# Optimization experiments

Hardware: AMD Instinct MI355X
Metric: run time of the kernel (lower is better)

## Reference

```python
import jax, jax.numpy as jnp
import numpy as np

DIM = 256
HEADS = 8
DIM_HEAD = 64
HIDDEN = HEADS * DIM_HEAD
SCALE = DIM_HEAD ** -0.5


def setup_inputs() -> dict:
    key = jax.random.key(0)
    ks = jax.random.split(key, 8)
    std = 0.02
    x = jax.random.normal(ks[0], (2, DIM, 16, 64, 64), dtype=jnp.float32)
    Wq = jax.random.normal(ks[1], (HIDDEN, DIM), dtype=jnp.float32) * std
    Wk = jax.random.normal(ks[2], (HIDDEN, DIM), dtype=jnp.float32) * std
    Wv = jax.random.normal(ks[3], (HIDDEN, DIM), dtype=jnp.float32) * std
    Wg = jax.random.normal(ks[4], (HIDDEN, DIM), dtype=jnp.float32) * std
    bg = jnp.zeros((HIDDEN,), dtype=jnp.float32)
    Wo = jax.random.normal(ks[5], (DIM, HIDDEN), dtype=jnp.float32) * std
    bo = jnp.zeros((DIM,), dtype=jnp.float32)
    return {"x": x, "Wq": Wq, "Wk": Wk, "Wv": Wv, "Wg": Wg, "bg": bg, "Wo": Wo, "bo": bo}


def _proj(x, W):  # 1x1 conv, no bias: (B,C,H,W) @ (O,C) -> (B,O,H,W)
    return jnp.einsum('bchw,oc->bohw', x, W)


def reference(x, Wq, Wk, Wv, Wg, bg, Wo, bo):
    b, c, f, h, w = x.shape
    xf = x.transpose(0, 2, 1, 3, 4).reshape(b * f, c, h, w)  # (bf, c, h, w)
    q = _proj(xf, Wq)
    k = _proj(xf, Wk)
    v = _proj(xf, Wv)
    g = _proj(xf, Wg) + bg[None, :, None, None]
    # softmax over height for q, width for k (pre-reshape, as in torch)
    q = jax.nn.softmax(q, axis=-2)
    k = jax.nn.softmax(k, axis=-1)

    def to_heads(t):  # (bf, H*D, h, w) -> (bf, H, h*w, D)
        return t.reshape(b * f, HEADS, DIM_HEAD, h * w).transpose(0, 1, 3, 2)

    q, k, v, g = map(to_heads, (q, k, v, g))
    q = jax.nn.elu(q) + 1.0
    k = jax.nn.elu(k) + 1.0
    g = jax.nn.sigmoid(g)

    kv = jnp.einsum('bhnd,bhne->bhde', k, v)
    k_sum = k.sum(axis=2)                                   # (bf, H, D)
    z = 1.0 / jnp.maximum(jnp.einsum('bhnd,bhd->bhn', q, k_sum), 1e-6)
    out = jnp.einsum('bhnd,bhde->bhne', q * SCALE, kv)
    out = out * z[..., None] * g                            # (bf, H, n, D)

    out = out.transpose(0, 1, 3, 2).reshape(b * f, HIDDEN, h, w)
    out = jnp.einsum('bchw,oc->bohw', out, Wo) + bo[None, :, None, None]
    return out.reshape(b, f, c, h, w).transpose(0, 2, 1, 3, 4)
```

## Files before the change

kernel.cpp:

```cpp
#include <hip/hip_runtime.h>


typedef unsigned short u16;
typedef unsigned int u32;
typedef __bf16 bf16x8 __attribute__((ext_vector_type(8)));
typedef float f32x4 __attribute__((ext_vector_type(4)));

typedef const __attribute__((address_space(1))) void* gas_t;
typedef __attribute__((address_space(3))) void* las_t;
__device__ __forceinline__ void gll16(const void* g, void* l) {
    __builtin_amdgcn_global_load_lds((gas_t)g, (las_t)l, 16, 0, 0);
}

__device__ inline float bf2f(u16 v) { union { u32 i; float f; } u; u.i = ((u32)v) << 16; return u.f; }
__device__ inline u16 f2bf(float f) {
    union { float f; u32 i; } u; u.f = f;
    u32 r = (u.i + 0x7fffu + ((u.i >> 16) & 1u)) >> 16;
    return (u16)r;
}
__device__ inline void split2(float v, u16& h, u16& l) {
    h = f2bf(v);
    l = f2bf(v - bf2f(h));
}

__global__ void k_cvt_w(const float* __restrict__ Wq, const float* __restrict__ Wk,
                        const float* __restrict__ Wv, const float* __restrict__ Wg,
                        const float* __restrict__ Wo,
                        u16* __restrict__ Wh, u16* __restrict__ Wl,
                        u16* __restrict__ Woh, u16* __restrict__ Wol)
{
    int idx = blockIdx.x * 256 + threadIdx.x;
    if (idx < 524288) {
        int o = idx >> 8, c = idx & 255;
        int which = o >> 9, r = o & 511;
        const float* s = (which == 0) ? Wq : (which == 1) ? Wk : (which == 2) ? Wv : Wg;
        u16 h, l; split2(s[r * 256 + c], h, l);
        Wh[idx] = h; Wl[idx] = l;
    } else {
        int j = idx - 524288;
        if (j < 131072) { u16 h, l; split2(Wo[j], h, l); Woh[j] = h; Wol[j] = l; }
    }
}

__global__ __launch_bounds__(256) void k_cvt_x(const float* __restrict__ x,
                                               u16* __restrict__ xh, u16* __restrict__ xl,
                                               int c0)
{
    __shared__ __align__(16) u16 tileh[64 * 132];
    __shared__ __align__(16) u16 tilel[64 * 132];
    const int t = threadIdx.x;
    const int bfl = blockIdx.y;
    const int bfg = c0 + bfl;
    const int n0 = blockIdx.x * 128;
    const int b_ = bfg >> 4, f_ = bfg & 15;
    for (int s = 0; s < 2; ++s) {
        for (int ch2 = 0; ch2 < 2; ++ch2) {
            __syncthreads();
            for (int p = 0; p < 8; ++p) {
                int cl = p * 16 + (t >> 4);
                int c = ch2 * 128 + cl;
                const float* sp = x + (((size_t)b_ * 256 + c) * 16 + f_) * 4096
                                    + n0 + s * 64 + (t & 15) * 4;
                float4 v = *(const float4*)sp;
                float vv[4] = { v.x, v.y, v.z, v.w };
#pragma unroll
                for (int j = 0; j < 4; ++j) {
                    int nl = (t & 15) * 4 + j;
                    u16 h, l; split2(vv[j], h, l);
                    tileh[nl * 132 + cl] = h;
                    tilel[nl * 132 + cl] = l;
                }
            }
            __syncthreads();
#pragma unroll
            for (int i = 0; i < 4; ++i) {
                int flat = t + i * 256;
                int nn = flat >> 4, cc = flat & 15;
                size_t off = ((size_t)bfl * 4096 + n0 + s * 64 + nn) * 256 + ch2 * 128 + cc * 8;
                *(uint4*)(xh + off) = *(const uint4*)(tileh + nn * 132 + cc * 8);
                *(uint4*)(xl + off) = *(const uint4*)(tilel + nn * 132 + cc * 8);
            }
        }
    }
}

__global__ __launch_bounds__(256) void k_proj(
    const u16* __restrict__ Wh, const u16* __restrict__ Wl,
    const u16* __restrict__ xh, const u16* __restrict__ xl,
    const float* __restrict__ bg,
    float* __restrict__ qf,
    u16* __restrict__ kh, u16* __restrict__ kl,
    u16* __restrict__ vh, u16* __restrict__ vl,
    float* __restrict__ gf)
{
    __shared__ __align__(16) char smem[65536];
    u16* Ah = (u16*)smem;
    u16* Al = (u16*)(smem + 16384);
    u16* Bh = (u16*)(smem + 32768);
    u16* Bl = (u16*)(smem + 49152);
    float* Csh = (float*)smem;
    const int t = threadIdx.x;
    const int bfl = blockIdx.z;
    const int by = blockIdx.y;
    const int m0 = (by < 4) ? by * 128 : 512 + (by - 4) * 128;
    const int n0 = blockIdx.x * 128;
    const int lane = t & 63, wv = t >> 6, wm = wv >> 1, wn = wv & 1;
    f32x4 acc[4][4] = {};
    const u16* Aph = Wh + (size_t)m0 * 256;
    const u16* Apl = Wl + (size_t)m0 * 256;
    const u16* Bph = xh + ((size_t)bfl * 4096 + n0) * 256;
    const u16* Bpl = xl + ((size_t)bfl * 4096 + n0) * 256;

    for (int kt = 0; kt < 4; ++kt) {
        const int k0 = kt * 64;
#pragma unroll
        for (int jj = 0; jj < 4; ++jj) {
            int s = wv * 4 + jj;
            int row = s * 8 + (lane >> 3);
            int csrc = (lane & 7) ^ (row & 7);
            size_t go = (size_t)row * 256 + k0 + csrc * 8;
            gll16(Aph + go, Ah + s * 512);
            gll16(Apl + go, Al + s * 512);
            gll16(Bph + go, Bh + s * 512);
            gll16(Bpl + go, Bl + s * 512);
        }
        __syncthreads();
#pragma unroll
        for (int kk = 0; kk < 2; ++kk) {
            bf16x8 afh[4], afl[4], bfh[4], bfl_[4];
#pragma unroll
            for (int i = 0; i < 4; ++i) {
                int ra = wm * 64 + i * 16 + (lane & 15);
                int ca = ((kk * 4 + (lane >> 4)) ^ (ra & 7)) * 8;
                afh[i] = *(const bf16x8*)(Ah + ra * 64 + ca);
                afl[i] = *(const bf16x8*)(Al + ra * 64 + ca);
                int rb = wn * 64 + i * 16 + (lane & 15);
                int cb = ((kk * 4 + (lane >> 4)) ^ (rb & 7)) * 8;
                bfh[i] = *(const bf16x8*)(Bh + rb * 64 + cb);
                bfl_[i] = *(const bf16x8*)(Bl + rb * 64 + cb);
            }
#pragma unroll
            for (int mi = 0; mi < 4; ++mi)
#pragma unroll
                for (int ni = 0; ni < 4; ++ni) {
                    acc[mi][ni] = __builtin_amdgcn_mfma_f32_16x16x32_bf16(afh[mi], bfh[ni], acc[mi][ni], 0, 0, 0);
                    acc[mi][ni] = __builtin_amdgcn_mfma_f32_16x16x32_bf16(afh[mi], bfl_[ni], acc[mi][ni], 0, 0, 0);
                    acc[mi][ni] = __builtin_amdgcn_mfma_f32_16x16x32_bf16(afl[mi], bfh[ni], acc[mi][ni], 0, 0, 0);
                }
        }
        __syncthreads();
    }

    const int sector = m0 >> 9;
    for (int ph = 0; ph < 2; ++ph) {
        if (wn == ph) {
#pragma unroll
            for (int mi = 0; mi < 4; ++mi)
#pragma unroll
                for (int ni = 0; ni < 4; ++ni)
#pragma unroll
                    for (int r = 0; r < 4; ++r) {
                        int gr = wm * 64 + mi * 16 + (lane >> 4) * 4 + r;
                        int gcl = ni * 16 + (lane & 15);
                        Csh[gr * 69 + gcl] = acc[mi][ni][r];
                    }
        }
        __syncthreads();
        if (sector == 0) {
#pragma unroll
            for (int rr = 0; rr < 2; ++rr) {
                int n_loc = rr * 32 + (t >> 3);
                int oct = t & 7;
                float* dst = qf + ((size_t)bfl * 4096 + n0 + ph * 64 + n_loc) * 512 + m0;
#pragma unroll
                for (int j = 0; j < 4; ++j) {
                    f32x4 o;
#pragma unroll
                    for (int c = 0; c < 4; ++c)
                        o[c] = Csh[(j * 32 + oct * 4 + c) * 69 + n_loc];
                    *(f32x4*)(dst + j * 32 + oct * 4) = o;
                }
            }
        } else if (t < 128) {
            const float* src = Csh + t * 69;
            const int oloc = (m0 & 511) + t;
            const size_t doff = ((size_t)bfl * 512 + oloc) * 4096 + n0 + ph * 64;
            if (sector == 2) {
#pragma unroll
                for (int i = 0; i < 8; ++i) {
                    union { u16 h[8]; uint4 u; } ph_, pl_;
#pragma unroll
                    for (int j = 0; j < 8; ++j) split2(src[i * 8 + j], ph_.h[j], pl_.h[j]);
                    *(uint4*)(vh + doff + i * 8) = ph_.u;
                    *(uint4*)(vl + doff + i * 8) = pl_.u;
                }
            } else if (sector == 1) {
                float mx = -3.0e38f;
                for (int j = 0; j < 64; ++j) mx = fmaxf(mx, src[j]);
                float sum = 0.f;
                for (int j = 0; j < 64; ++j) sum += expf(src[j] - mx);
                float rs = 1.0f / sum;
#pragma unroll
                for (int i = 0; i < 8; ++i) {
                    union { u16 h[8]; uint4 u; } ph_, pl_;
#pragma unroll
                    for (int j = 0; j < 8; ++j) {
                        float p = expf(src[i * 8 + j] - mx) * rs;
                        split2(p, ph_.h[j], pl_.h[j]);
                    }
                    *(uint4*)(kh + doff + i * 8) = ph_.u;
                    *(uint4*)(kl + doff + i * 8) = pl_.u;
                }
            } else {
                float bgv = bg[oloc];
#pragma unroll
                for (int i = 0; i < 16; ++i) {
                    float4 o;
                    float* po = (float*)&o;
#pragma unroll
                    for (int j = 0; j < 4; ++j)
                        po[j] = 1.0f / (1.0f + expf(-(src[i * 4 + j] + bgv)));
                    *(float4*)(gf + doff + i * 4) = o;
                }
            }
        }
        __syncthreads();
    }
}

__global__ __launch_bounds__(256) void k_smq(
    const float* __restrict__ qf, u16* __restrict__ qTh, u16* __restrict__ qTl)
{
    __shared__ float S[4 * 64 * 64];
    const int t = threadIdx.x;
    const int wblk = blockIdx.x;
    const int bh = blockIdx.y;
    const int bfl = bh >> 3, head = bh & 7;
    const float* qbase = qf + (size_t)bfl * 4096 * 512 + head * 64;
#pragma unroll
    for (int r = 0; r < 16; ++r) {
        int h = r * 4 + (t >> 6);
        int w = (t >> 4) & 3;
        int li = t & 15;
        f32x4 v = *(const f32x4*)(qbase + (size_t)(h * 64 + wblk * 4 + w) * 512 + li * 4);
        *(f32x4*)(S + ((w * 64 + h) * 64 + li * 4)) = v;
    }
    __syncthreads();
    {
        int w = t >> 6, d = t & 63;
        float mx = -3.0e38f;
        for (int h = 0; h < 64; ++h) mx = fmaxf(mx, S[(w * 64 + h) * 64 + d]);
        float sum = 0.f;
        for (int h = 0; h < 64; ++h) {
            int i = (w * 64 + h) * 64 + d;
            float e = expf(S[i] - mx);
            S[i] = e;
            sum += e;
        }
        float rs = 1.0f / sum;
        for (int h = 0; h < 64; ++h) S[(w * 64 + h) * 64 + d] *= rs;
    }
    __syncthreads();
#pragma unroll
    for (int r = 0; r < 8; ++r) {
        int px = r * 32 + (t >> 3);
        int h = px >> 2, w = px & 3;
        int oct = t & 7;
        union { u16 h16[8]; uint4 u; } ph_, pl_;
#pragma unroll
        for (int j = 0; j < 8; ++j)
            split2(S[(w * 64 + h) * 64 + oct * 8 + j], ph_.h16[j], pl_.h16[j]);
        size_t off = ((size_t)bh * 4096 + h * 64 + wblk * 4 + w) * 64 + oct * 8;
        *(uint4*)(qTh + off) = ph_.u;
        *(uint4*)(qTl + off) = pl_.u;
    }
}

__global__ __launch_bounds__(256) void k_kv(
    const u16* __restrict__ kh, const u16* __restrict__ kl,
    const u16* __restrict__ vh, const u16* __restrict__ vl,
    float* __restrict__ kvp, float* __restrict__ vsp, float* __restrict__ ksp)
{
    __shared__ __align__(16) char smem[65536];
    u16* Kh = (u16*)smem;
    u16* Kl = (u16*)(smem + 16384);
    u16* Vh = (u16*)(smem + 32768);
    u16* Vl = (u16*)(smem + 49152);
    float* mrg = (float*)smem;
    const int t = threadIdx.x;
    const int oct = blockIdx.x;
    const int bh = blockIdx.y;
    const int NBH = gridDim.y;
    const int lane = t & 63, wv = t >> 6;
    const size_t hb = (size_t)bh * 64 * 4096;

    f32x4 acc[5][5] = {};
    bf16x8 ones;
#pragma unroll
    for (int j = 0; j < 8; ++j) ones[j] = (lane & 15) == 0 ? (__bf16)1.0f : (__bf16)0.0f;

    for (int cc = 0; cc < 4; ++cc) {
        const int pxc = oct * 512 + cc * 128;
#pragma unroll
        for (int jj = 0; jj < 4; ++jj) {
            int s = wv * 4 + jj;
            int row = s * 4 + (lane >> 4);
            int csrc = (lane & 15) ^ (row & 7);
            size_t go = hb + (size_t)row * 4096 + pxc + csrc * 8;
            gll16(kh + go, Kh + s * 512);
            gll16(kl + go, Kl + s * 512);
            gll16(vh + go, Vh + s * 512);
            gll16(vl + go, Vl + s * 512);
        }
        __syncthreads();
        bf16x8 ah[4], al[4], bh_[4], bl_[4];
#pragma unroll
        for (int i = 0; i < 4; ++i) {
            int ra = i * 16 + (lane & 15);
            int kc = (wv * 4 + (lane >> 4)) ^ (ra & 7);
            int off = ra * 128 + kc * 8;
            ah[i]  = *(const bf16x8*)(Kh + off);
            al[i]  = *(const bf16x8*)(Kl + off);
            bh_[i] = *(const bf16x8*)(Vh + off);
            bl_[i] = *(const bf16x8*)(Vl + off);
        }
#pragma unroll
        for (int di = 0; di < 5; ++di) {
            bf16x8 a = (di < 4) ? ah[di] : ones;
#pragma unroll
            for (int ei = 0; ei < 5; ++ei) {
                bf16x8 b = (ei < 4) ? bh_[ei] : ones;
                acc[di][ei] = __builtin_amdgcn_mfma_f32_16x16x32_bf16(a, b, acc[di][ei], 0, 0, 0);
            }
        }
#pragma unroll
        for (int di = 0; di < 5; ++di) {
            bf16x8 a = (di < 4) ? ah[di] : ones;
#pragma unroll
            for (int ei = 0; ei < 4; ++ei)
                acc[di][ei] = __builtin_amdgcn_mfma_f32_16x16x32_bf16(a, bl_[ei], acc[di][ei], 0, 0, 0);
        }
#pragma unroll
        for (int di = 0; di < 4; ++di)
#pragma unroll
            for (int ei = 0; ei < 5; ++ei) {
                bf16x8 b = (ei < 4) ? bh_[ei] : ones;
                acc[di][ei] = __builtin_amdgcn_mfma_f32_16x16x32_bf16(al[di], b, acc[di][ei], 0, 0, 0);
            }
        __syncthreads();
    }

    float* kvm = mrg;
    float* vsm = mrg + 64 * 68;
    float* ksm = mrg + 64 * 68 + 64;
    for (int i = t; i < 64 * 68 + 128; i += 256) mrg[i] = 0.f;
    __syncthreads();
#pragma unroll
    for (int di = 0; di < 4; ++di)
#pragma unroll
        for (int ei = 0; ei < 4; ++ei)
#pragma unroll
            for (int r = 0; r < 4; ++r) {
                int d = di * 16 + (lane >> 4) * 4 + r;
                int e = ei * 16 + (lane & 15);
                atomicAdd(&kvm[d * 68 + e], acc[di][ei][r]);
            }
    if (lane < 16) {
#pragma unroll
        for (int ei = 0; ei < 4; ++ei) atomicAdd(&vsm[ei * 16 + lane], acc[4][ei][0]);
    }
    if ((lane & 15) == 0) {
#pragma unroll
        for (int di = 0; di < 4; ++di)
#pragma unroll
            for (int r = 0; r < 4; ++r)
                atomicAdd(&ksm[di * 16 + (lane >> 4) * 4 + r], acc[di][4][r]);
    }
    __syncthreads();
    float* op = kvp + ((size_t)oct * NBH + bh) * 4096;
#pragma unroll
    for (int i = 0; i < 16; ++i) {
        int idx = t + i * 256;
        op[idx] = kvm[(idx >> 6) * 68 + (idx & 63)];
    }
    if (t < 64) {
        vsp[((size_t)oct * NBH + bh) * 64 + t] = vsm[t];
        ksp[((size_t)oct * NBH + bh) * 64 + t] = 512.0f + ksm[t];
    }
}

__global__ __launch_bounds__(256) void k_merge(
    const float* __restrict__ kvp, const float* __restrict__ vsp,
    const float* __restrict__ ksp,
    u16* __restrict__ kvTh, u16* __restrict__ kvTl,
    float* __restrict__ aux, int NBH)
{
    __shared__ float kv[64 * 68];
    __shared__ float vsl[64];
    __shared__ float kslL[64];
    const int t = threadIdx.x;
    const int bh = blockIdx.x;
#pragma unroll
    for (int i = 0; i < 16; ++i) {
        int idx = t + i * 256;
        float s = 0.f;
#pragma unroll
        for (int o = 0; o < 8; ++o) s += kvp[((size_t)o * NBH + bh) * 4096 + idx];
        kv[(idx >> 6) * 68 + (idx & 63)] = s;
    }
    if (t < 64) {
        float a = 0.f, b = 0.f;
#pragma unroll
        for (int o = 0; o < 8; ++o) {
            a += vsp[((size_t)o * NBH + bh) * 64 + t];
            b += ksp[((size_t)o * NBH + bh) * 64 + t];
        }
        vsl[t] = a; kslL[t] = b;
    }
    __syncthreads();
    if (t < 64) {
        float s = 0.f;
        for (int d = 0; d < 64; ++d) s += kv[d * 68 + t];
        aux[(size_t)bh * 68 + t] = s + 64.0f * vsl[t];
    }
    if (t == 64) {
        float s = 0.f;
        for (int d = 0; d < 64; ++d) s += kslL[d];
        aux[(size_t)bh * 68 + 64] = s;
    }
    __syncthreads();
    {
        int m = t >> 2, kq = t & 3;
        union { u16 h[16]; uint4 u[2]; } hh, ll;
        float vm = vsl[m];
#pragma unroll
        for (int i = 0; i < 16; ++i) {
            int k = kq * 16 + i;
            split2(kv[k * 68 + m] + vm, hh.h[i], ll.h[i]);
        }
        size_t off = (size_t)bh * 5120 + (size_t)m * 64 + kq * 16;
        *(uint4*)(kvTh + off) = hh.u[0];
        *(uint4*)(kvTh + off + 8) = hh.u[1];
        *(uint4*)(kvTl + off) = ll.u[0];
        *(uint4*)(kvTl + off + 8) = ll.u[1];
    }
    if (t < 64) {
        int m2 = 64 + (t >> 2), kq = t & 3;
        union { u16 h[16]; uint4 u[2]; } hh, ll;
#pragma unroll
        for (int i = 0; i < 16; ++i) {
            float v = (m2 == 64) ? kslL[kq * 16 + i] : 0.f;
            split2(v, hh.h[i], ll.h[i]);
        }
        size_t off = (size_t)bh * 5120 + (size_t)m2 * 64 + kq * 16;
        *(uint4*)(kvTh + off) = hh.u[0];
        *(uint4*)(kvTh + off + 8) = hh.u[1];
        *(uint4*)(kvTl + off) = ll.u[0];
        *(uint4*)(kvTl + off + 8) = ll.u[1];
    }
}

__global__ __launch_bounds__(256) void k_att(
    const u16* __restrict__ qTh_g, const u16* __restrict__ qTl_g,
    const float* __restrict__ gf,
    const u16* __restrict__ kvTh_g, const u16* __restrict__ kvTl_g,
    const float* __restrict__ aux,
    u16* __restrict__ atth, u16* __restrict__ attl)
{
    __shared__ __align__(16) char smem[71680];
    u16* qh_s = (u16*)smem;
    u16* ql_s = (u16*)(smem + 32768);
    u16* ah_s = (u16*)smem;
    u16* al_s = (u16*)(smem + 34816);
    float* szl = (float*)(smem + 69632);
    float* cslL = (float*)(smem + 70656);
    const int t = threadIdx.x;
    const int lane = t & 63, wv = t >> 6;
    const int row = lane & 15, oct = lane >> 4;
    const int bh = blockIdx.y;
    const int bfl = bh >> 3, head = bh & 7;
    const int n0 = blockIdx.x * 256;

    const u16* qhb = qTh_g + ((size_t)bh * 4096 + n0) * 64;
    const u16* qlb = qTl_g + ((size_t)bh * 4096 + n0) * 64;
#pragma unroll
    for (int r = 0; r < 8; ++r) {
        int chunk = r * 256 + t;
        int n = chunk >> 3, c = chunk & 7;
        size_t src = (size_t)n * 64 + (size_t)((c ^ (n & 7)) * 8);
        gll16(qhb + src, qh_s + r * 2048 + wv * 512);
        gll16(qlb + src, ql_s + r * 2048 + wv * 512);
    }
    if (t < 65) cslL[t] = aux[(size_t)bh * 68 + t];
    __syncthreads();

    f32x4 acc[5][4] = {};
    const u16* Ahg = kvTh_g + (size_t)bh * 5120;
    const u16* Alg = kvTl_g + (size_t)bh * 5120;
#pragma unroll
    for (int pass = 0; pass < 3; ++pass) {
        const u16* Ap = (pass == 2) ? Alg : Ahg;
        const u16* Bp = (pass == 1) ? ql_s : qh_s;
#pragma unroll
        for (int ks = 0; ks < 2; ++ks) {
            bf16x8 af[5], bq[4];
#pragma unroll
            for (int mi = 0; mi < 5; ++mi)
                af[mi] = *(const bf16x8*)(Ap + (size_t)(mi * 16 + row) * 64 + ks * 32 + oct * 8);
#pragma unroll
            for (int ni = 0; ni < 4; ++ni) {
                int n_loc = wv * 64 + ni * 16 + row;
                int chs = ((ks * 4 + oct) ^ (n_loc & 7)) * 8;
                bq[ni] = *(const bf16x8*)(Bp + n_loc * 64 + chs);
            }
#pragma unroll
            for (int mi = 0; mi < 5; ++mi)
#pragma unroll
                for (int ni = 0; ni < 4; ++ni)
                    acc[mi][ni] = __builtin_amdgcn_mfma_f32_16x16x32_bf16(af[mi], bq[ni], acc[mi][ni], 0, 0, 0);
        }
    }
    if (oct == 0) {
#pragma unroll
        for (int ni = 0; ni < 4; ++ni)
            szl[wv * 64 + ni * 16 + row] = acc[4][ni][0];
    }
    __syncthreads();

    const float kstp = cslL[64];
#pragma unroll
    for (int ni = 0; ni < 4; ++ni) {
        int n_loc = wv * 64 + ni * 16 + row;
        int n_g = n0 + n_loc;
        float zz = 0.125f / fmaxf(szl[n_loc] + kstp, 1e-6f);
#pragma unroll
        for (int mi = 0; mi < 4; ++mi) {
            int e0 = mi * 16 + oct * 4;
            u16 hh[4], ll2[4];
#pragma unroll
            for (int r2 = 0; r2 < 4; ++r2) {
                int e = e0 + r2;
                float g = gf[((size_t)bfl * 512 + head * 64 + e) * 4096 + n_g];
                float val = (acc[mi][ni][r2] + cslL[e]) * zz * g;
                split2(val, hh[r2], ll2[r2]);
            }
            *(u32*)(ah_s + n_loc * 68 + e0)     = (u32)hh[0] | ((u32)hh[1] << 16);
            *(u32*)(ah_s + n_loc * 68 + e0 + 2) = (u32)hh[2] | ((u32)hh[3] << 16);
            *(u32*)(al_s + n_loc * 68 + e0)     = (u32)ll2[0] | ((u32)ll2[1] << 16);
            *(u32*)(al_s + n_loc * 68 + e0 + 2) = (u32)ll2[2] | ((u32)ll2[3] << 16);
        }
    }
    __syncthreads();
    u16* gh = atth + ((size_t)bfl * 4096 + n0) * 512 + head * 64;
    u16* gl = attl + ((size_t)bfl * 4096 + n0) * 512 + head * 64;
#pragma unroll
    for (int r = 0; r < 16; ++r) {
        int n_loc = r * 16 + (t >> 4);
        int u2 = t & 15;
        *(uint2*)(gh + (size_t)n_loc * 512 + u2 * 4) = *(const uint2*)(ah_s + n_loc * 68 + u2 * 4);
        *(uint2*)(gl + (size_t)n_loc * 512 + u2 * 4) = *(const uint2*)(al_s + n_loc * 68 + u2 * 4);
    }
}

__global__ __launch_bounds__(256) void k_out(
    const u16* __restrict__ Woh, const u16* __restrict__ Wol,
    const u16* __restrict__ atth, const u16* __restrict__ attl,
    const float* __restrict__ bo, float* __restrict__ out, int c0)
{
    __shared__ __align__(16) u16 smem[32768];
    u16* Ah = smem;
    u16* Al = smem + 8192;
    u16* Bh = smem + 16384;
    u16* Bl = smem + 24576;
    const int t = threadIdx.x;
    const int bfl = blockIdx.z;
    const int bfg = c0 + bfl;
    const int m0 = blockIdx.y * 128;
    const int n0 = blockIdx.x * 128;
    const int lane = t & 63, wv = t >> 6, wm = wv >> 1, wn = wv & 1;
    f32x4 acc[4][4] = {};
    const u16* Aph = Woh + (size_t)m0 * 512;
    const u16* Apl = Wol + (size_t)m0 * 512;
    const u16* Bph = atth + ((size_t)bfl * 4096 + n0) * 512;
    const u16* Bpl = attl + ((size_t)bfl * 4096 + n0) * 512;
    for (int kt = 0; kt < 8; ++kt) {
        const int k0 = kt * 64;
#pragma unroll
        for (int jj = 0; jj < 4; ++jj) {
            int s = wv * 4 + jj;
            int row = s * 8 + (lane >> 3);
            int csrc = (lane & 7) ^ (row & 7);
            size_t go = (size_t)row * 512 + k0 + csrc * 8;
            gll16(Aph + go, Ah + s * 512);
            gll16(Apl + go, Al + s * 512);
            gll16(Bph + go, Bh + s * 512);
            gll16(Bpl + go, Bl + s * 512);
        }
        __syncthreads();
#pragma unroll
        for (int kk = 0; kk < 2; ++kk) {
            bf16x8 afh[4], afl[4], bfh[4], bfl_[4];
#pragma unroll
            for (int i = 0; i < 4; ++i) {
                int ra = wm * 64 + i * 16 + (lane & 15);
                int ca = ((kk * 4 + (lane >> 4)) ^ (ra & 7)) * 8;
                afh[i] = *(const bf16x8*)(Ah + ra * 64 + ca);
                afl[i] = *(const bf16x8*)(Al + ra * 64 + ca);
                int rb = wn * 64 + i * 16 + (lane & 15);
                int cb = ((kk * 4 + (lane >> 4)) ^ (rb & 7)) * 8;
                bfh[i] = *(const bf16x8*)(Bh + rb * 64 + cb);
                bfl_[i] = *(const bf16x8*)(Bl + rb * 64 + cb);
            }
#pragma unroll
            for (int mi = 0; mi < 4; ++mi)
#pragma unroll
                for (int ni = 0; ni < 4; ++ni) {
                    acc[mi][ni] = __builtin_amdgcn_mfma_f32_16x16x32_bf16(afh[mi], bfh[ni], acc[mi][ni], 0, 0, 0);
                    acc[mi][ni] = __builtin_amdgcn_mfma_f32_16x16x32_bf16(afh[mi], bfl_[ni], acc[mi][ni], 0, 0, 0);
                    acc[mi][ni] = __builtin_amdgcn_mfma_f32_16x16x32_bf16(afl[mi], bfh[ni], acc[mi][ni], 0, 0, 0);
                }
        }
        __syncthreads();
    }
    const int b_ = bfg >> 4, f_ = bfg & 15;
#pragma unroll
    for (int mi = 0; mi < 4; ++mi)
#pragma unroll
        for (int ni = 0; ni < 4; ++ni)
#pragma unroll
            for (int r = 0; r < 4; ++r) {
                int o = m0 + wm * 64 + mi * 16 + (lane >> 4) * 4 + r;
                int nn = n0 + wn * 64 + ni * 16 + (lane & 15);
                out[(((size_t)b_ * 256 + o) * 16 + f_) * 4096 + nn] = acc[mi][ni][r] + bo[o];
            }
}

extern "C" void kernel_launch(void* const* d_in, const int* in_sizes, int n_in,
                              void* d_out, int out_size, void* d_ws, size_t ws_size,
                              hipStream_t stream)
{
    const float* x  = (const float*)d_in[0];
    const float* Wq = (const float*)d_in[1];
    const float* Wk = (const float*)d_in[2];
    const float* Wv = (const float*)d_in[3];
    const float* Wg = (const float*)d_in[4];
    const float* bg = (const float*)d_in[5];
    const float* Wo = (const float*)d_in[6];
    const float* bo = (const float*)d_in[7];
    float* out = (float*)d_out;
    char* ws = (char*)d_ws;

    const size_t PER_BF = 47386624ull;
    const size_t FIXED  = 2621440ull;
    int CH = 32;
    while (CH > 1 && FIXED + (size_t)CH * PER_BF > ws_size) CH >>= 1;
    const int nch = 32 / CH;

    u16* Wh  = (u16*)(ws);
    u16* Wl  = (u16*)(ws + 1048576);
    u16* Woh = (u16*)(ws + 2097152);
    u16* Wol = (u16*)(ws + 2359296);
    char* dyn = ws + FIXED;
    u16*   xh   = (u16*)(dyn);
    u16*   xl   = (u16*)(dyn + (size_t)CH * 2097152);
    u16*   kh   = (u16*)(dyn + (size_t)CH * 4194304);
    u16*   kl   = (u16*)(dyn + (size_t)CH * 8388608);
    u16*   vh   = (u16*)(dyn + (size_t)CH * 12582912);
    u16*   vl   = (u16*)(dyn + (size_t)CH * 16777216);
    float* qf   = (float*)(dyn + (size_t)CH * 20971520);
    float* gf   = (float*)(dyn + (size_t)CH * 29360128);
    u16*   qTh  = (u16*)(dyn + (size_t)CH * 37748736);
    u16*   qTl  = (u16*)(dyn + (size_t)CH * 41943040);
    float* kvp  = (float*)(dyn + (size_t)CH * 46137344);
    float* vsp  = (float*)(dyn + (size_t)CH * 47185920);
    float* ksp  = (float*)(dyn + (size_t)CH * 47202304);
    u16*   kvTh = (u16*)(dyn + (size_t)CH * 47218688);
    u16*   kvTl = (u16*)(dyn + (size_t)CH * 47300608);
    float* aux  = (float*)(dyn + (size_t)CH * 47382528);
    u16*   atth = kh;
    u16*   attl = kl;

    k_cvt_w<<<dim3(2560), dim3(256), 0, stream>>>(Wq, Wk, Wv, Wg, Wo, Wh, Wl, Woh, Wol);

    for (int c = 0; c < nch; ++c) {
        const int c0 = c * CH;
        k_cvt_x<<<dim3(32, CH),     dim3(256), 0, stream>>>(x, xh, xl, c0);
        k_proj <<<dim3(32, 16, CH), dim3(256), 0, stream>>>(Wh, Wl, xh, xl, bg,
                                                            qf, kh, kl, vh, vl, gf);
        k_kv   <<<dim3(8, CH * 8),  dim3(256), 0, stream>>>(kh, kl, vh, vl, kvp, vsp, ksp);
        k_merge<<<dim3(CH * 8),     dim3(256), 0, stream>>>(kvp, vsp, ksp, kvTh, kvTl, aux, CH * 8);
        k_smq  <<<dim3(16, CH * 8), dim3(256), 0, stream>>>(qf, qTh, qTl);
        k_att  <<<dim3(16, CH * 8), dim3(256), 0, stream>>>(qTh, qTl, gf, kvTh, kvTl, aux, atth, attl);
        k_out  <<<dim3(32, 2, CH),  dim3(256), 0, stream>>>(Woh, Wol, atth, attl, bo, out, c0);
    }
}
```

Before: 1.751 ms.

## Fuse q softmax into attention kernel and halve k_proj LDS tile depth

Removes the standalone k_smq kernel. The height softmax on q and its bf16 hi/lo split now run inside the attention kernel, so the qTh/qTl intermediate buffers are no longer written or re-read. The gate is now written pixel-major, the same layout as q, so the attention kernel reads it with vector loads instead of strided scalar loads. k_proj's K-tile drops from 64 to 32 with a new swizzle, cutting shared memory from 64KB to about 36KB, likely for higher occupancy. The fused kernel adds extra barriers, and its softmax uses only 128 threads doing serial loops.

Measured after the change: 1.779 ms. Within noise of the previous version (+1.6%).

```diff
diff --git a/kernel.cpp b/kernel.cpp
--- a/kernel.cpp
+++ b/kernel.cpp
@@ -93,11 +93,11 @@
     u16* __restrict__ vh, u16* __restrict__ vl,
     float* __restrict__ gf)
 {
-    __shared__ __align__(16) char smem[65536];
+    __shared__ __align__(16) char smem[36352];
     u16* Ah = (u16*)smem;
-    u16* Al = (u16*)(smem + 16384);
-    u16* Bh = (u16*)(smem + 32768);
-    u16* Bl = (u16*)(smem + 49152);
+    u16* Al = (u16*)(smem + 8192);
+    u16* Bh = (u16*)(smem + 16384);
+    u16* Bl = (u16*)(smem + 24576);
     float* Csh = (float*)smem;
     const int t = threadIdx.x;
     const int bfl = blockIdx.z;
@@ -111,13 +111,13 @@
     const u16* Bph = xh + ((size_t)bfl * 4096 + n0) * 256;
     const u16* Bpl = xl + ((size_t)bfl * 4096 + n0) * 256;
 
-    for (int kt = 0; kt < 4; ++kt) {
-        const int k0 = kt * 64;
-#pragma unroll
-        for (int jj = 0; jj < 4; ++jj) {
-            int s = wv * 4 + jj;
-            int row = s * 8 + (lane >> 3);
-            int csrc = (lane & 7) ^ (row & 7);
+    for (int kt = 0; kt < 8; ++kt) {
+        const int k0 = kt * 32;
+#pragma unroll
+        for (int jj = 0; jj < 2; ++jj) {
+            int s = wv * 2 + jj;
+            int row = s * 16 + (lane >> 2);
+            int csrc = (lane & 3) ^ ((row >> 1) & 3);
             size_t go = (size_t)row * 256 + k0 + csrc * 8;
             gll16(Aph + go, Ah + s * 512);
             gll16(Apl + go, Al + s * 512);
@@ -125,29 +125,26 @@
             gll16(Bpl + go, Bl + s * 512);
         }
         __syncthreads();
-#pragma unroll
-        for (int kk = 0; kk < 2; ++kk) {
-            bf16x8 afh[4], afl[4], bfh[4], bfl_[4];
-#pragma unroll
-            for (int i = 0; i < 4; ++i) {
-                int ra = wm * 64 + i * 16 + (lane & 15);
-                int ca = ((kk * 4 + (lane >> 4)) ^ (ra & 7)) * 8;
-                afh[i] = *(const bf16x8*)(Ah + ra * 64 + ca);
-                afl[i] = *(const bf16x8*)(Al + ra * 64 + ca);
-                int rb = wn * 64 + i * 16 + (lane & 15);
-                int cb = ((kk * 4 + (lane >> 4)) ^ (rb & 7)) * 8;
-                bfh[i] = *(const bf16x8*)(Bh + rb * 64 + cb);
-                bfl_[i] = *(const bf16x8*)(Bl + rb * 64 + cb);
-            }
-#pragma unroll
-            for (int mi = 0; mi < 4; ++mi)
-#pragma unroll
-                for (int ni = 0; ni < 4; ++ni) {
-                    acc[mi][ni] = __builtin_amdgcn_mfma_f32_16x16x32_bf16(afh[mi], bfh[ni], acc[mi][ni], 0, 0, 0);
-                    acc[mi][ni] = __builtin_amdgcn_mfma_f32_16x16x32_bf16(afh[mi], bfl_[ni], acc[mi][ni], 0, 0, 0);
-                    acc[mi][ni] = __builtin_amdgcn_mfma_f32_16x16x32_bf16(afl[mi], bfh[ni], acc[mi][ni], 0, 0, 0);
-                }
-        }
+        bf16x8 afh[4], afl[4], bfh[4], bfl_[4];
+#pragma unroll
+        for (int i = 0; i < 4; ++i) {
+            int ra = wm * 64 + i * 16 + (lane & 15);
+            int ca = ((lane >> 4) ^ ((ra >> 1) & 3)) * 8;
+            afh[i] = *(const bf16x8*)(Ah + ra * 32 + ca);
+            afl[i] = *(const bf16x8*)(Al + ra * 32 + ca);
+            int rb = wn * 64 + i * 16 + (lane & 15);
+            int cb = ((lane >> 4) ^ ((rb >> 1) & 3)) * 8;
+            bfh[i] = *(const bf16x8*)(Bh + rb * 32 + cb);
+            bfl_[i] = *(const bf16x8*)(Bl + rb * 32 + cb);
+        }
+#pragma unroll
+        for (int mi = 0; mi < 4; ++mi)
+#pragma unroll
+            for (int ni = 0; ni < 4; ++ni) {
+                acc[mi][ni] = __builtin_amdgcn_mfma_f32_16x16x32_bf16(afh[mi], bfh[ni], acc[mi][ni], 0, 0, 0);
+                acc[mi][ni] = __builtin_amdgcn_mfma_f32_16x16x32_bf16(afh[mi], bfl_[ni], acc[mi][ni], 0, 0, 0);
+                acc[mi][ni] = __builtin_amdgcn_mfma_f32_16x16x32_bf16(afl[mi], bfh[ni], acc[mi][ni], 0, 0, 0);
+            }
         __syncthreads();
     }
 
@@ -166,19 +163,25 @@
                     }
         }
         __syncthreads();
-        if (sector == 0) {
+        if (sector == 0 || sector == 3) {
+            float* dstbuf = (sector == 0) ? qf : gf;
+            const int cbase = m0 & 511;
 #pragma unroll
             for (int rr = 0; rr < 2; ++rr) {
                 int n_loc = rr * 32 + (t >> 3);
-                int oct = t & 7;
-                float* dst = qf + ((size_t)bfl * 4096 + n0 + ph * 64 + n_loc) * 512 + m0;
+                int oc = t & 7;
+                float* dst = dstbuf + ((size_t)bfl * 4096 + n0 + ph * 64 + n_loc) * 512 + cbase;
 #pragma unroll
                 for (int j = 0; j < 4; ++j) {
                     f32x4 o;
 #pragma unroll
-                    for (int c = 0; c < 4; ++c)
-                        o[c] = Csh[(j * 32 + oct * 4 + c) * 69 + n_loc];
-                    *(f32x4*)(dst + j * 32 + oct * 4) = o;
+                    for (int c = 0; c < 4; ++c) {
+                        float v = Csh[(j * 32 + oc * 4 + c) * 69 + n_loc];
+                        if (sector == 3)
+                            v = 1.0f / (1.0f + expf(-(v + bg[cbase + j * 32 + oc * 4 + c])));
+                        o[c] = v;
+                    }
+                    *(f32x4*)(dst + j * 32 + oc * 4) = o;
                 }
             }
         } else if (t < 128) {
@@ -194,7 +197,7 @@
                     *(uint4*)(vh + doff + i * 8) = ph_.u;
                     *(uint4*)(vl + doff + i * 8) = pl_.u;
                 }
-            } else if (sector == 1) {
+            } else {
                 float mx = -3.0e38f;
                 for (int j = 0; j < 64; ++j) mx = fmaxf(mx, src[j]);
                 float sum = 0.f;
@@ -211,68 +214,9 @@
                     *(uint4*)(kh + doff + i * 8) = ph_.u;
                     *(uint4*)(kl + doff + i * 8) = pl_.u;
                 }
-            } else {
-                float bgv = bg[oloc];
-#pragma unroll
-                for (int i = 0; i < 16; ++i) {
-                    float4 o;
-                    float* po = (float*)&o;
-#pragma unroll
-                    for (int j = 0; j < 4; ++j)
-                        po[j] = 1.0f / (1.0f + expf(-(src[i * 4 + j] + bgv)));
-                    *(float4*)(gf + doff + i * 4) = o;
-                }
-            }
-        }
-        __syncthreads();
-    }
-}
-
-__global__ __launch_bounds__(256) void k_smq(
-    const float* __restrict__ qf, u16* __restrict__ qTh, u16* __restrict__ qTl)
-{
-    __shared__ float S[4 * 64 * 64];
-    const int t = threadIdx.x;
-    const int wblk = blockIdx.x;
-    const int bh = blockIdx.y;
-    const int bfl = bh >> 3, head = bh & 7;
-    const float* qbase = qf + (size_t)bfl * 4096 * 512 + head * 64;
-#pragma unroll
-    for (int r = 0; r < 16; ++r) {
-        int h = r * 4 + (t >> 6);
-        int w = (t >> 4) & 3;
-        int li = t & 15;
-        f32x4 v = *(const f32x4*)(qbase + (size_t)(h * 64 + wblk * 4 + w) * 512 + li * 4);
-        *(f32x4*)(S + ((w * 64 + h) * 64 + li * 4)) = v;
-    }
-    __syncthreads();
-    {
-        int w = t >> 6, d = t & 63;
-        float mx = -3.0e38f;
-        for (int h = 0; h < 64; ++h) mx = fmaxf(mx, S[(w * 64 + h) * 64 + d]);
-        float sum = 0.f;
-        for (int h = 0; h < 64; ++h) {
-            int i = (w * 64 + h) * 64 + d;
-            float e = expf(S[i] - mx);
-            S[i] = e;
-            sum += e;
-        }
-        float rs = 1.0f / sum;
-        for (int h = 0; h < 64; ++h) S[(w * 64 + h) * 64 + d] *= rs;
-    }
-    __syncthreads();
-#pragma unroll
-    for (int r = 0; r < 8; ++r) {
-        int px = r * 32 + (t >> 3);
-        int h = px >> 2, w = px & 3;
-        int oct = t & 7;
-        union { u16 h16[8]; uint4 u; } ph_, pl_;
-#pragma unroll
-        for (int j = 0; j < 8; ++j)
-            split2(S[(w * 64 + h) * 64 + oct * 8 + j], ph_.h16[j], pl_.h16[j]);
-        size_t off = ((size_t)bh * 4096 + h * 64 + wblk * 4 + w) * 64 + oct * 8;
-        *(uint4*)(qTh + off) = ph_.u;
-        *(uint4*)(qTl + off) = pl_.u;
+            }
+        }
+        __syncthreads();
     }
 }
 
@@ -460,65 +404,79 @@
     }
 }
 
-__global__ __launch_bounds__(256) void k_att(
-    const u16* __restrict__ qTh_g, const u16* __restrict__ qTl_g,
-    const float* __restrict__ gf,
+__global__ __launch_bounds__(256) void k_smatt(
+    const float* __restrict__ qf, const float* __restrict__ gf,
     const u16* __restrict__ kvTh_g, const u16* __restrict__ kvTl_g,
     const float* __restrict__ aux,
     u16* __restrict__ atth, u16* __restrict__ attl)
 {
     __shared__ __align__(16) char smem[71680];
-    u16* qh_s = (u16*)smem;
-    u16* ql_s = (u16*)(smem + 32768);
-    u16* ah_s = (u16*)smem;
-    u16* al_s = (u16*)(smem + 34816);
-    float* szl = (float*)(smem + 69632);
+    float* qS   = (float*)smem;
+    u16* fragH  = (u16*)(smem + 32768);
+    u16* fragL  = (u16*)(smem + 49152);
+    u16* ah_s   = (u16*)smem;
+    u16* al_s   = (u16*)(smem + 34816);
+    float* szl  = (float*)(smem + 69632);
     float* cslL = (float*)(smem + 70656);
     const int t = threadIdx.x;
     const int lane = t & 63, wv = t >> 6;
     const int row = lane & 15, oct = lane >> 4;
     const int bh = blockIdx.y;
     const int bfl = bh >> 3, head = bh & 7;
-    const int n0 = blockIdx.x * 256;
-
-    const u16* qhb = qTh_g + ((size_t)bh * 4096 + n0) * 64;
-    const u16* qlb = qTl_g + ((size_t)bh * 4096 + n0) * 64;
-#pragma unroll
-    for (int r = 0; r < 8; ++r) {
-        int chunk = r * 256 + t;
-        int n = chunk >> 3, c = chunk & 7;
-        size_t src = (size_t)n * 64 + (size_t)((c ^ (n & 7)) * 8);
-        gll16(qhb + src, qh_s + r * 2048 + wv * 512);
-        gll16(qlb + src, ql_s + r * 2048 + wv * 512);
-    }
+    const int w0 = blockIdx.x * 4;
+
     if (t < 65) cslL[t] = aux[(size_t)bh * 68 + t];
-    __syncthreads();
 
     f32x4 acc[5][4] = {};
     const u16* Ahg = kvTh_g + (size_t)bh * 5120;
     const u16* Alg = kvTl_g + (size_t)bh * 5120;
-#pragma unroll
-    for (int pass = 0; pass < 3; ++pass) {
-        const u16* Ap = (pass == 2) ? Alg : Ahg;
-        const u16* Bp = (pass == 1) ? ql_s : qh_s;
-#pragma unroll
-        for (int ks = 0; ks < 2; ++ks) {
+    const float* qbase = qf + ((size_t)bfl * 4096) * 512 + head * 64;
+
+    for (int ks = 0; ks < 2; ++ks) {
+#pragma unroll
+        for (int r = 0; r < 8; ++r) {
+            int px = r * 32 + wv * 8 + (lane >> 3);
+            int c  = lane & 7;
+            int ng = (px & 63) * 64 + w0 + (px >> 6);
+            gll16(qbase + (size_t)ng * 512 + ks * 32 + c * 4,
+                  (char*)smem + r * 4096 + wv * 1024);
+        }
+        __syncthreads();
+        if (t < 128) {
+            int w = t >> 5, d = t & 31;
+            const float* col = qS + (w * 64) * 32 + d;
+            float mx = -3.0e38f;
+            for (int h = 0; h < 64; ++h) mx = fmaxf(mx, col[h * 32]);
+            float sum = 0.f;
+            for (int h = 0; h < 64; ++h) sum += expf(col[h * 32] - mx);
+            float rs = 1.0f / sum;
+            for (int h = 0; h < 64; ++h) {
+                float p = expf(col[h * 32] - mx) * rs;
+                u16 hh, ll;
+                split2(p, hh, ll);
+                fragH[(w * 64 + h) * 32 + d] = hh;
+                fragL[(w * 64 + h) * 32 + d] = ll;
+            }
+        }
+        __syncthreads();
+#pragma unroll
+        for (int pass = 0; pass < 3; ++pass) {
+            const u16* Ap = (pass == 2) ? Alg : Ahg;
+            const u16* Bp = (pass == 1) ? fragL : fragH;
             bf16x8 af[5], bq[4];
 #pragma unroll
             for (int mi = 0; mi < 5; ++mi)
                 af[mi] = *(const bf16x8*)(Ap + (size_t)(mi * 16 + row) * 64 + ks * 32 + oct * 8);
 #pragma unroll
-            for (int ni = 0; ni < 4; ++ni) {
-                int n_loc = wv * 64 + ni * 16 + row;
-                int chs = ((ks * 4 + oct) ^ (n_loc & 7)) * 8;
-                bq[ni] = *(const bf16x8*)(Bp + n_loc * 64 + chs);
-            }
+            for (int ni = 0; ni < 4; ++ni)
+                bq[ni] = *(const bf16x8*)(Bp + (wv * 64 + ni * 16 + row) * 32 + oct * 8);
 #pragma unroll
             for (int mi = 0; mi < 5; ++mi)
 #pragma unroll
                 for (int ni = 0; ni < 4; ++ni)
                     acc[mi][ni] = __builtin_amdgcn_mfma_f32_16x16x32_bf16(af[mi], bq[ni], acc[mi][ni], 0, 0, 0);
         }
+        __syncthreads();
     }
     if (oct == 0) {
 #pragma unroll
@@ -531,17 +489,18 @@
 #pragma unroll
     for (int ni = 0; ni < 4; ++ni) {
         int n_loc = wv * 64 + ni * 16 + row;
-        int n_g = n0 + n_loc;
+        int n_g = (n_loc & 63) * 64 + w0 + (n_loc >> 6);
         float zz = 0.125f / fmaxf(szl[n_loc] + kstp, 1e-6f);
+        const float* gp = gf + ((size_t)bfl * 4096 + n_g) * 512 + head * 64;
 #pragma unroll
         for (int mi = 0; mi < 4; ++mi) {
             int e0 = mi * 16 + oct * 4;
+            f32x4 g4 = *(const f32x4*)(gp + e0);
             u16 hh[4], ll2[4];
 #pragma unroll
             for (int r2 = 0; r2 < 4; ++r2) {
                 int e = e0 + r2;
-                float g = gf[((size_t)bfl * 512 + head * 64 + e) * 4096 + n_g];
-                float val = (acc[mi][ni][r2] + cslL[e]) * zz * g;
+                float val = (acc[mi][ni][r2] + cslL[e]) * zz * g4[r2];
                 split2(val, hh[r2], ll2[r2]);
             }
             *(u32*)(ah_s + n_loc * 68 + e0)     = (u32)hh[0] | ((u32)hh[1] << 16);
@@ -551,14 +510,15 @@
         }
     }
     __syncthreads();
-    u16* gh = atth + ((size_t)bfl * 4096 + n0) * 512 + head * 64;
-    u16* gl = attl + ((size_t)bfl * 4096 + n0) * 512 + head * 64;
+    u16* gh = atth + ((size_t)bfl * 4096) * 512 + head * 64;
+    u16* gl = attl + ((size_t)bfl * 4096) * 512 + head * 64;
 #pragma unroll
     for (int r = 0; r < 16; ++r) {
         int n_loc = r * 16 + (t >> 4);
         int u2 = t & 15;
-        *(uint2*)(gh + (size_t)n_loc * 512 + u2 * 4) = *(const uint2*)(ah_s + n_loc * 68 + u2 * 4);
-        *(uint2*)(gl + (size_t)n_loc * 512 + u2 * 4) = *(const uint2*)(al_s + n_loc * 68 + u2 * 4);
+        int n_g = (n_loc & 63) * 64 + w0 + (n_loc >> 6);
+        *(uint2*)(gh + (size_t)n_g * 512 + u2 * 4) = *(const uint2*)(ah_s + n_loc * 68 + u2 * 4);
+        *(uint2*)(gl + (size_t)n_g * 512 + u2 * 4) = *(const uint2*)(al_s + n_loc * 68 + u2 * 4);
     }
 }
 
@@ -650,7 +610,7 @@
     float* out = (float*)d_out;
     char* ws = (char*)d_ws;
 
-    const size_t PER_BF = 47386624ull;
+    const size_t PER_BF = 38996096ull;
     const size_t FIXED  = 2621440ull;
     int CH = 32;
     while (CH > 1 && FIXED + (size_t)CH * PER_BF > ws_size) CH >>= 1;
@@ -669,14 +629,12 @@
     u16*   vl   = (u16*)(dyn + (size_t)CH * 16777216);
     float* qf   = (float*)(dyn + (size_t)CH * 20971520);
     float* gf   = (float*)(dyn + (size_t)CH * 29360128);
-    u16*   qTh  = (u16*)(dyn + (size_t)CH * 37748736);
-    u16*   qTl  = (u16*)(dyn + (size_t)CH * 41943040);
-    float* kvp  = (float*)(dyn + (size_t)CH * 46137344);
-    float* vsp  = (float*)(dyn + (size_t)CH * 47185920);
-    float* ksp  = (float*)(dyn + (size_t)CH * 47202304);
-    u16*   kvTh = (u16*)(dyn + (size_t)CH * 47218688);
-    u16*   kvTl = (u16*)(dyn + (size_t)CH * 47300608);
-    float* aux  = (float*)(dyn + (size_t)CH * 47382528);
+    float* kvp  = (float*)(dyn + (size_t)CH * 37748736);
+    float* vsp  = (float*)(dyn + (size_t)CH * 38797312);
+    float* ksp  = (float*)(dyn + (size_t)CH * 38813696);
+    u16*   kvTh = (u16*)(dyn + (size_t)CH * 38830080);
+    u16*   kvTl = (u16*)(dyn + (size_t)CH * 38912000);
+    float* aux  = (float*)(dyn + (size_t)CH * 38993920);
     u16*   atth = kh;
     u16*   attl = kl;
 
@@ -689,8 +647,7 @@
                                                             qf, kh, kl, vh, vl, gf);
         k_kv   <<<dim3(8, CH * 8),  dim3(256), 0, stream>>>(kh, kl, vh, vl, kvp, vsp, ksp);
         k_merge<<<dim3(CH * 8),     dim3(256), 0, stream>>>(kvp, vsp, ksp, kvTh, kvTl, aux, CH * 8);
-        k_smq  <<<dim3(16, CH * 8), dim3(256), 0, stream>>>(qf, qTh, qTl);
-        k_att  <<<dim3(16, CH * 8), dim3(256), 0, stream>>>(qTh, qTl, gf, kvTh, kvTl, aux, atth, attl);
+        k_smatt<<<dim3(16, CH * 8), dim3(256), 0, stream>>>(qf, gf, kvTh, kvTl, aux, atth, attl);
         k_out  <<<dim3(32, 2, CH),  dim3(256), 0, stream>>>(Woh, Wol, atth, attl, bo, out, c0);
     }
 }
```
